# Kernel optimization log

Measured on AMD Instinct MI355X. Metric: run time of the kernel, lower is better.

Reference implementation:

```python
import jax, jax.numpy as jnp
import numpy as np

# dims: O=1 templates/chains, L=384 residues, d_pair=d_bias=128, 4 heads x 32
O, L, DP, DB, H, DH = 1, 384, 128, 128, 4, 32
SCALING = 1.0 / np.sqrt(DH)


def _ln(x, g, b):
    # torch nn.LayerNorm over last dim, eps=1e-5, biased variance
    m = jnp.mean(x, axis=-1, keepdims=True)
    v = jnp.mean((x - m) ** 2, axis=-1, keepdims=True)
    return (x - m) * jax.lax.rsqrt(v + 1e-5) * g + b


def setup_inputs() -> dict:
    key = jax.random.key(0)
    ks = jax.random.split(key, 9)

    def w(k, shape, s=0.02):
        return (jax.random.normal(k, shape) * s).astype(jnp.float32)

    return {
        "pair": jax.random.normal(ks[0], (O, L, L, DP), dtype=jnp.float32),
        "bias": jax.random.normal(ks[1], (O, L, L, DB), dtype=jnp.float32),
        "ln_pair_g": jnp.ones((DP,), jnp.float32),
        "ln_pair_b": jnp.zeros((DP,), jnp.float32),
        "ln_bias_g": jnp.ones((DB,), jnp.float32),
        "ln_bias_b": jnp.zeros((DB,), jnp.float32),
        "Wq": w(ks[2], (H * DH, DP)),  # torch Linear weight layout (out, in)
        "Wk": w(ks[3], (H * DH, DP)),
        "Wv": w(ks[4], (H * DH, DP)),
        "Wb": w(ks[5], (H, DB)),
        "Wg": w(ks[6], (H * DH, DP)),
        "bg": jnp.ones((H * DH,), jnp.float32),
        "Wo": w(ks[7], (DP, H * DH)),
        "bo": w(ks[8], (DP,)),
    }


def reference(pair, bias, ln_pair_g, ln_pair_b, ln_bias_g, ln_bias_b,
              Wq, Wk, Wv, Wb, Wg, bg, Wo, bo):
    # is_row=True: swap the two L axes so attention runs along rows
    p = jnp.transpose(pair, (0, 2, 1, 3))   # [O, L, L, DP]
    bsrc = jnp.transpose(bias, (0, 2, 1, 3))  # [O, L, L, DB]

    p = _ln(p, ln_pair_g, ln_pair_b)
    bsrc = _ln(bsrc, ln_bias_g, ln_bias_b)

    q = (p @ Wq.T).reshape(O, L, L, H, DH) * SCALING
    k = (p @ Wk.T).reshape(O, L, L, H, DH) / L
    v = (p @ Wv.T).reshape(O, L, L, H, DH)
    b = bsrc @ Wb.T                         # [O, L, L, H] pairwise bias
    gate = jax.nn.sigmoid(p @ Wg.T + bg)    # [O, L, L, H*DH]

    # attention scores contracted over the non-attended axial dim n and head dim k
    attn = jnp.einsum('bnihk,bnjhk->bijh', q, k) + b
    attn = jax.nn.softmax(attn, axis=2)     # softmax over j (torch dim=-2)

    out = jnp.einsum('bijh,bnjhd->bnihd', attn, v).reshape(O, L, L, H * DH)
    out = (gate * out) @ Wo.T + bo          # [O, L, L, DP]
    return jnp.transpose(out, (0, 2, 1, 3))  # undo is_row permute
```

## Files before the change

### kernel.cpp

```cpp
#include <hip/hip_runtime.h>
#include <hip/hip_bf16.h>

#define L_DIM 384
#define DPC 128
#define NH 4
#define DHD 32
#define HD 128
#define NROWS (L_DIM*L_DIM)
#define NSPLIT 16

typedef __hip_bfloat16 bf16;
typedef __attribute__((ext_vector_type(8))) short bf8_t;
typedef __attribute__((ext_vector_type(4))) short bf4_t;
typedef __attribute__((ext_vector_type(4))) float f4_t;

__device__ __forceinline__ float bf2f(bf16 x){ return __bfloat162float(x); }
__device__ __forceinline__ bf16 f2bf(float x){ return __float2bfloat16(x); }

union bfu8 { bf8_t v; bf16 h[8]; };

__global__ __launch_bounds__(256) void k_prep(
    const float* __restrict__ Wq, const float* __restrict__ Wk, const float* __restrict__ Wv,
    const float* __restrict__ Wg, const float* __restrict__ Wo,
    bf16* __restrict__ Wqp, bf16* __restrict__ Wkp, bf16* __restrict__ Wvp,
    bf16* __restrict__ Wgp, bf16* __restrict__ Wop)
{
  const int o = blockIdx.x * 256 + threadIdx.x;
  const int j = o & 7, lane = (o >> 3) & 63, ks = (o >> 9) & 3, nt = o >> 11;
  const int src = (nt*16 + (lane & 15))*DPC + ks*32 + (lane >> 4)*8 + j;
  Wqp[o] = f2bf(Wq[src]);
  Wkp[o] = f2bf(Wk[src]);
  Wvp[o] = f2bf(Wv[src]);
  Wgp[o] = f2bf(Wg[src]);
  Wop[o] = f2bf(Wo[src]);
}

__global__ __launch_bounds__(256) void k_bias_proj(
    const float* __restrict__ bias, const float* __restrict__ lng, const float* __restrict__ lnb,
    const float* __restrict__ Wb, float* __restrict__ bscore)
{
  const int tid = threadIdx.x;
  const int wave = tid >> 6, lane = tid & 63;
  const int sub = lane >> 4, l16 = lane & 15, c = l16 * 8;
  const int t = blockIdx.x * 16 + wave * 4 + sub;
  const int j = t / L_DIM, i = t % L_DIM;

  const float4 ga = *(const float4*)&lng[c], gb = *(const float4*)&lng[c+4];
  const float4 ba = *(const float4*)&lnb[c], bb = *(const float4*)&lnb[c+4];
  const float4 xa = *(const float4*)&bias[(size_t)t * DPC + c];
  const float4 xb = *(const float4*)&bias[(size_t)t * DPC + c + 4];

  float s  = xa.x+xa.y+xa.z+xa.w + xb.x+xb.y+xb.z+xb.w;
  float ss = xa.x*xa.x+xa.y*xa.y+xa.z*xa.z+xa.w*xa.w
           + xb.x*xb.x+xb.y*xb.y+xb.z*xb.z+xb.w*xb.w;
  #pragma unroll
  for (int off = 8; off; off >>= 1) { s += __shfl_xor(s, off, 64); ss += __shfl_xor(ss, off, 64); }
  const float mean = s * (1.f/128.f);
  const float var  = ss * (1.f/128.f) - mean*mean;
  const float rstd = rsqrtf(var + 1e-5f);
  float y[8];
  y[0]=(xa.x-mean)*rstd*ga.x+ba.x; y[1]=(xa.y-mean)*rstd*ga.y+ba.y;
  y[2]=(xa.z-mean)*rstd*ga.z+ba.z; y[3]=(xa.w-mean)*rstd*ga.w+ba.w;
  y[4]=(xb.x-mean)*rstd*gb.x+bb.x; y[5]=(xb.y-mean)*rstd*gb.y+bb.y;
  y[6]=(xb.z-mean)*rstd*gb.z+bb.z; y[7]=(xb.w-mean)*rstd*gb.w+bb.w;

  float p[4];
  #pragma unroll
  for (int h = 0; h < 4; ++h) {
    const float4 wa = *(const float4*)&Wb[h*DPC + c];
    const float4 wb4 = *(const float4*)&Wb[h*DPC + c + 4];
    p[h] = y[0]*wa.x + y[1]*wa.y + y[2]*wa.z + y[3]*wa.w
         + y[4]*wb4.x + y[5]*wb4.y + y[6]*wb4.z + y[7]*wb4.w;
    #pragma unroll
    for (int off = 8; off; off >>= 1) p[h] += __shfl_xor(p[h], off, 64);
  }
  if (l16 == 0) {
    #pragma unroll
    for (int h = 0; h < 4; ++h)
      bscore[((size_t)h*L_DIM + i)*L_DIM + j] = p[h];
  }
}

__global__ __launch_bounds__(256) void k_pair_proj(
    const float* __restrict__ pair, const float* __restrict__ lng, const float* __restrict__ lnb,
    const bf16* __restrict__ Wqp, const bf16* __restrict__ Wkp, const bf16* __restrict__ Wvp,
    const bf16* __restrict__ Wgp, const float* __restrict__ bg,
    bf16* __restrict__ qf, bf16* __restrict__ kf, bf16* __restrict__ vf, bf16* __restrict__ gatef)
{
  __shared__ __align__(16) bf16 Sh[5120];
  const int tid = threadIdx.x;
  const int wave = tid >> 6, lane = tid & 63;
  const int n = blockIdx.x / 12, i0 = (blockIdx.x % 12) * 32;
  const int m = lane & 15, q4 = lane >> 4;
  const int rt = wave >> 1, ch = wave & 1;

  {
    const int half = lane >> 5, l32 = lane & 31, c = l32 * 4;
    const float4 g4 = *(const float4*)&lng[c];
    const float4 b4 = *(const float4*)&lnb[c];
    float4 xv[4];
    #pragma unroll
    for (int rr = 0; rr < 4; ++rr) {
      int r = wave*8 + rr*2 + half;
      xv[rr] = *(const float4*)&pair[((size_t)(i0 + r)*L_DIM + n)*DPC + c];
    }
    #pragma unroll
    for (int rr = 0; rr < 4; ++rr) {
      int r = wave*8 + rr*2 + half;
      float s  = xv[rr].x + xv[rr].y + xv[rr].z + xv[rr].w;
      float ss = xv[rr].x*xv[rr].x + xv[rr].y*xv[rr].y + xv[rr].z*xv[rr].z + xv[rr].w*xv[rr].w;
      #pragma unroll
      for (int off = 16; off; off >>= 1) { s += __shfl_xor(s, off, 64); ss += __shfl_xor(ss, off, 64); }
      float mean = s * (1.f/128.f);
      float var  = ss * (1.f/128.f) - mean*mean;
      float rstd = rsqrtf(var + 1e-5f);
      union { bf16 h[4]; bf4_t v; } pk;
      pk.h[0] = f2bf((xv[rr].x-mean)*rstd*g4.x + b4.x);
      pk.h[1] = f2bf((xv[rr].y-mean)*rstd*g4.y + b4.y);
      pk.h[2] = f2bf((xv[rr].z-mean)*rstd*g4.z + b4.z);
      pk.h[3] = f2bf((xv[rr].w-mean)*rstd*g4.w + b4.w);
      *(bf4_t*)&Sh[r*136 + c] = pk.v;
    }
  }
  __syncthreads();

  bf8_t afr[4];
  #pragma unroll
  for (int ks = 0; ks < 4; ++ks)
    afr[ks] = *(const bf8_t*)&Sh[(rt*16 + m)*136 + ks*32 + q4*8];
  __syncthreads();

  const bf16* Ws[4] = {Wqp, Wkp, Wvp, Wgp};
  for (int sel = 0; sel < 4; ++sel) {
    const bf16* Wp = Ws[sel];
    #pragma unroll
    for (int ntl = 0; ntl < 4; ++ntl) {
      const int nt = ch*4 + ntl;
      f4_t acc = {0.f, 0.f, 0.f, 0.f};
      #pragma unroll
      for (int ks = 0; ks < 4; ++ks) {
        bf8_t bfr = *(const bf8_t*)&Wp[(nt*4 + ks)*512 + lane*8];
        acc = __builtin_amdgcn_mfma_f32_16x16x32_bf16(afr[ks], bfr, acc, 0, 0, 0);
      }
      const int col = nt*16 + m;
      if (sel == 2) {
        #pragma unroll
        for (int reg = 0; reg < 4; ++reg)
          Sh[col*40 + rt*16 + q4*4 + reg] = f2bf(acc[reg]);
      } else {
        const float bgv = (sel == 3) ? bg[col] : 0.f;
        #pragma unroll
        for (int reg = 0; reg < 4; ++reg) {
          float v = acc[reg];
          if (sel == 3) v = 1.f / (1.f + __expf(-(v + bgv)));
          Sh[(rt*16 + q4*4 + reg)*136 + col] = f2bf(v);
        }
      }
    }
    __syncthreads();
    if (sel == 2) {
      for (int u = tid; u < 512; u += 256) {
        int ln = u & 63, dt = (u >> 6) & 1, h = u >> 7;
        bf8_t val = *(const bf8_t*)&Sh[(h*32 + dt*16 + (ln&15))*40 + (ln>>4)*8];
        size_t dst = ((((size_t)n*NH + h)*12 + (i0>>5))*2 + dt)*512 + (size_t)ln*8;
        *(bf8_t*)&vf[dst] = val;
      }
    } else {
      for (int u = tid; u < 512; u += 256) {
        int Il = u >> 8, h = (u >> 6) & 3, ln = u & 63;
        bf8_t val = *(const bf8_t*)&Sh[(Il*16 + (ln&15))*136 + h*32 + (ln>>4)*8];
        if (sel == 3) {
          size_t dst = ((((size_t)n*24 + (i0>>4) + Il)*NH + h)*64 + ln)*8;
          *(bf8_t*)&gatef[dst] = val;
        } else {
          bf16* out = (sel == 0) ? qf : kf;
          size_t dst = ((((size_t)n*NH + h)*24 + (i0>>4) + Il)*64 + ln)*8;
          *(bf8_t*)&out[dst] = val;
        }
      }
    }
    __syncthreads();
  }
}

__global__ __launch_bounds__(256) void k_qk(
    const bf16* __restrict__ qf, const bf16* __restrict__ kf, float* __restrict__ Spart)
{
  const int tid = threadIdx.x, wave = tid >> 6, lane = tid & 63;
  const int m = lane & 15, q4 = lane >> 4;
  const int b = blockIdx.x;
  const int ks = b / 36, rem = b % 36;
  const int h = rem / 9, t9 = rem % 9;
  const int i0 = (t9/3)*128, j0 = (t9%3)*128;
  const int wr = (wave >> 1)*64, wc = (wave & 1)*64;

  f4_t acc[4][4];
  #pragma unroll
  for (int a = 0; a < 4; ++a)
    #pragma unroll
    for (int c = 0; c < 4; ++c) acc[a][c] = (f4_t){0.f,0.f,0.f,0.f};

  #pragma unroll 2
  for (int kt = 0; kt < 24; ++kt) {
    const int nIdx = ks*24 + kt;
    const bf16* qb = qf + (((size_t)nIdx*NH + h)*24 + ((i0 + wr) >> 4))*512;
    const bf16* kb = kf + (((size_t)nIdx*NH + h)*24 + ((j0 + wc) >> 4))*512;
    bf8_t af[4], bfr[4];
    #pragma unroll
    for (int x = 0; x < 4; ++x) {
      af[x]  = *(const bf8_t*)&qb[x*512 + lane*8];
      bfr[x] = *(const bf8_t*)&kb[x*512 + lane*8];
    }
    #pragma unroll
    for (int mt = 0; mt < 4; ++mt)
      #pragma unroll
      for (int nt = 0; nt < 4; ++nt)
        acc[mt][nt] = __builtin_amdgcn_mfma_f32_16x16x32_bf16(af[mt], bfr[nt], acc[mt][nt], 0, 0, 0);
  }
  float* Sp = Spart + (size_t)(ks*NH + h)*L_DIM*L_DIM;
  #pragma unroll
  for (int mt = 0; mt < 4; ++mt)
    #pragma unroll
    for (int nt = 0; nt < 4; ++nt)
      #pragma unroll
      for (int reg = 0; reg < 4; ++reg) {
        int i = i0 + wr + mt*16 + q4*4 + reg;
        int j = j0 + wc + nt*16 + m;
        Sp[(size_t)i*L_DIM + j] = acc[mt][nt][reg];
      }
}

__global__ __launch_bounds__(192) void k_softmax(
    const float* __restrict__ Spart, const float* __restrict__ bscore, bf16* __restrict__ attnf)
{
  const int t = threadIdx.x, wave = t >> 6, lane = t & 63;
  const int h = blockIdx.x / L_DIM, i = blockIdx.x % L_DIM;
  const float sc = 0.17677669529663687f / 384.f;
  const size_t off = ((size_t)h*L_DIM + i)*L_DIM + t*2;

  float ax = 0.f, ay = 0.f;
  #pragma unroll
  for (int ksp = 0; ksp < NSPLIT; ++ksp) {
    float2 p = *(const float2*)&Spart[(size_t)ksp*(NH*L_DIM*L_DIM) + off];
    ax += p.x; ay += p.y;
  }
  const float2 bs = *(const float2*)&bscore[off];
  ax = ax*sc + bs.x;
  ay = ay*sc + bs.y;

  __shared__ float redm[3], reds[3];
  float mx = fmaxf(ax, ay);
  #pragma unroll
  for (int o = 32; o; o >>= 1) mx = fmaxf(mx, __shfl_xor(mx, o, 64));
  if (lane == 0) redm[wave] = mx;
  __syncthreads();
  mx = fmaxf(fmaxf(redm[0], redm[1]), redm[2]);
  float ex = __expf(ax - mx), ey = __expf(ay - mx);
  float sm = ex + ey;
  #pragma unroll
  for (int o = 32; o; o >>= 1) sm += __shfl_xor(sm, o, 64);
  if (lane == 0) reds[wave] = sm;
  __syncthreads();
  const float inv = 1.f / (reds[0] + reds[1] + reds[2]);

  const int j = t*2;
  const int I = i >> 4, mm = i & 15, J = j >> 5, q4 = (j >> 3) & 3, jj = j & 7;
  union { bf16 h2[2]; unsigned u; } pk;
  pk.h2[0] = f2bf(ex * inv);
  pk.h2[1] = f2bf(ey * inv);
  size_t a = ((((size_t)h*24 + I)*12 + J)*64 + q4*16 + mm)*8 + jj;
  *(unsigned*)&attnf[a] = pk.u;
}

__global__ __launch_bounds__(256) void k_pv(
    const bf16* __restrict__ attnf, const bf16* __restrict__ vf, const bf16* __restrict__ gatef,
    bf16* __restrict__ goutf)
{
  __shared__ __align__(16) bf16 Cs2[384*40];
  const int tid = threadIdx.x, wave = tid >> 6, lane = tid & 63;
  const int m = lane & 15, q4 = lane >> 4;
  const int n = blockIdx.x >> 2, h = blockIdx.x & 3;

  f4_t acc[6][2];
  #pragma unroll
  for (int a = 0; a < 6; ++a) { acc[a][0] = (f4_t){0,0,0,0}; acc[a][1] = (f4_t){0,0,0,0}; }

  for (int J = 0; J < 12; ++J) {
    const bf16* vb = vf + (((size_t)(n*NH + h)*12 + J)*2)*512;
    bf8_t b0 = *(const bf8_t*)&vb[lane*8];
    bf8_t b1 = *(const bf8_t*)&vb[512 + lane*8];
    #pragma unroll
    for (int mt = 0; mt < 6; ++mt) {
      const int I = wave*6 + mt;
      bf8_t af = *(const bf8_t*)&attnf[(((size_t)h*24 + I)*12 + J)*512 + (size_t)lane*8];
      acc[mt][0] = __builtin_amdgcn_mfma_f32_16x16x32_bf16(af, b0, acc[mt][0], 0, 0, 0);
      acc[mt][1] = __builtin_amdgcn_mfma_f32_16x16x32_bf16(af, b1, acc[mt][1], 0, 0, 0);
    }
  }
  #pragma unroll
  for (int mt = 0; mt < 6; ++mt)
    #pragma unroll
    for (int dt = 0; dt < 2; ++dt)
      #pragma unroll
      for (int reg = 0; reg < 4; ++reg) {
        int i_loc = 16*(wave*6 + mt) + q4*4 + reg;
        Cs2[i_loc*40 + dt*16 + m] = f2bf(acc[mt][dt][reg]);
      }
  __syncthreads();
  #pragma unroll
  for (int it = 0; it < 6; ++it) {
    int u = tid + it*256;
    int I = u >> 6, ln = u & 63;
    bfu8 uc, ug, uo;
    uc.v = *(const bf8_t*)&Cs2[(I*16 + (ln&15))*40 + (ln>>4)*8];
    size_t gidx = ((((size_t)n*24 + I)*NH + h)*64 + ln)*8;
    ug.v = *(const bf8_t*)&gatef[gidx];
    #pragma unroll
    for (int e = 0; e < 8; ++e) uo.h[e] = f2bf(bf2f(uc.h[e]) * bf2f(ug.h[e]));
    *(bf8_t*)&goutf[gidx] = uo.v;
  }
}

__global__ __launch_bounds__(256) void k_out(
    const bf16* __restrict__ goutf, const bf16* __restrict__ Wop, const float* __restrict__ bo,
    float* __restrict__ outp)
{
  __shared__ __align__(16) float Cs[64][132];
  const int tid = threadIdx.x, wave = tid >> 6, lane = tid & 63;
  const int m = lane & 15, q4 = lane >> 4;
  const int n = blockIdx.x / 6, i0 = (blockIdx.x % 6) * 64;

  bf8_t afr[4];
  #pragma unroll
  for (int ks = 0; ks < 4; ++ks)
    afr[ks] = *(const bf8_t*)&goutf[((((size_t)n*24 + (i0>>4) + wave)*NH + ks)*64 + lane)*8];

  #pragma unroll
  for (int nt = 0; nt < 8; ++nt) {
    f4_t acc = {0.f, 0.f, 0.f, 0.f};
    #pragma unroll
    for (int ks = 0; ks < 4; ++ks) {
      bf8_t bfr = *(const bf8_t*)&Wop[(nt*4 + ks)*512 + lane*8];
      acc = __builtin_amdgcn_mfma_f32_16x16x32_bf16(afr[ks], bfr, acc, 0, 0, 0);
    }
    const int col = nt*16 + m;
    const float bov = bo[col];
    #pragma unroll
    for (int reg = 0; reg < 4; ++reg)
      Cs[wave*16 + q4*4 + reg][col] = acc[reg] + bov;
  }
  __syncthreads();
  for (int u = tid; u < 2048; u += 256) {
    int r = u >> 5, c4 = (u & 31) * 4;
    size_t off = ((size_t)(i0 + r)*L_DIM + n)*DPC + c4;
    *(float4*)&outp[off] = *(const float4*)&Cs[r][c4];
  }
}

extern "C" void kernel_launch(void* const* d_in, const int* in_sizes, int n_in,
                              void* d_out, int out_size, void* d_ws, size_t ws_size,
                              hipStream_t stream)
{
  (void)in_sizes; (void)n_in; (void)out_size; (void)ws_size;
  const float* pair = (const float*)d_in[0];
  const float* bias = (const float*)d_in[1];
  const float* lnpg = (const float*)d_in[2];
  const float* lnpb = (const float*)d_in[3];
  const float* lnbg = (const float*)d_in[4];
  const float* lnbb = (const float*)d_in[5];
  const float* Wq   = (const float*)d_in[6];
  const float* Wk   = (const float*)d_in[7];
  const float* Wv   = (const float*)d_in[8];
  const float* Wb   = (const float*)d_in[9];
  const float* Wg   = (const float*)d_in[10];
  const float* bg   = (const float*)d_in[11];
  const float* Wo   = (const float*)d_in[12];
  const float* bo   = (const float*)d_in[13];
  float* outp = (float*)d_out;

  char* ws = (char*)d_ws;
  const size_t SZ = (size_t)NROWS * HD * 2;
  bf16* qfb   = (bf16*)(ws);
  bf16* kfb   = (bf16*)(ws + SZ);
  bf16* vfb   = (bf16*)(ws + 2*SZ);
  bf16* gatef = (bf16*)(ws + 3*SZ);
  float* bscore = (float*)(ws + 4*SZ);
  float* Spart  = (float*)(ws + 4*SZ + (size_t)NH*L_DIM*L_DIM*4);
  bf16*  attnf  = (bf16*)(ws + 4*SZ + (size_t)NH*L_DIM*L_DIM*4 + (size_t)NSPLIT*NH*L_DIM*L_DIM*4);
  char*  wb     = ws + 4*SZ + (size_t)NH*L_DIM*L_DIM*4 + (size_t)NSPLIT*NH*L_DIM*L_DIM*4
                     + (size_t)NH*L_DIM*L_DIM*2;
  bf16* Wqp = (bf16*)(wb);
  bf16* Wkp = (bf16*)(wb + 32768);
  bf16* Wvp = (bf16*)(wb + 65536);
  bf16* Wgp = (bf16*)(wb + 98304);
  bf16* Wop = (bf16*)(wb + 131072);
  bf16* goutf = qfb;

  hipLaunchKernelGGL(k_prep, dim3(64), dim3(256), 0, stream, Wq, Wk, Wv, Wg, Wo,
                     Wqp, Wkp, Wvp, Wgp, Wop);
  hipLaunchKernelGGL(k_bias_proj, dim3(NROWS/16), dim3(256), 0, stream, bias, lnbg, lnbb, Wb, bscore);
  hipLaunchKernelGGL(k_pair_proj, dim3(NROWS/32), dim3(256), 0, stream, pair, lnpg, lnpb,
                     Wqp, Wkp, Wvp, Wgp, bg, qfb, kfb, vfb, gatef);
  hipLaunchKernelGGL(k_qk, dim3(NSPLIT*36), dim3(256), 0, stream, qfb, kfb, Spart);
  hipLaunchKernelGGL(k_softmax, dim3(NH*L_DIM), dim3(192), 0, stream, Spart, bscore, attnf);
  hipLaunchKernelGGL(k_pv, dim3(L_DIM*NH), dim3(256), 0, stream, attnf, vfb, gatef, goutf);
  hipLaunchKernelGGL(k_out, dim3(NROWS/64), dim3(256), 0, stream, goutf, Wop, bo, outp);
}
```

Before: 396.8 us.

## Batch projection stores, prefetch QK fragments, and preload gate in PV kernel

The pair projection kernel now computes Q, K and gate into three separate shared-memory buffers with no barriers between them, then computes V into the reused LN buffer. All global stores are issued in one final pass, which cuts the number of __syncthreads from about eight to three. The QK kernel double-buffers its per-iteration fragment loads so the next tile's global reads overlap the current tile's MFMAs. The PV kernel issues its gate loads before the main loop to hide their latency. In exchange, shared memory per block and register pressure go up, which may lower occupancy.

```diff
diff --git a/kernel.cpp b/kernel.cpp
--- a/kernel.cpp
+++ b/kernel.cpp
@@ -87,7 +87,11 @@
     const bf16* __restrict__ Wgp, const float* __restrict__ bg,
     bf16* __restrict__ qf, bf16* __restrict__ kf, bf16* __restrict__ vf, bf16* __restrict__ gatef)
 {
-  __shared__ __align__(16) bf16 Sh[5120];
+  __shared__ __align__(16) bf16 Sh[5120 + 3*4352];
+  bf16* AsCT = Sh;
+  bf16* Csq  = Sh + 5120;
+  bf16* Csk  = Sh + 5120 + 4352;
+  bf16* Csg  = Sh + 5120 + 2*4352;
   const int tid = threadIdx.x;
   const int wave = tid >> 6, lane = tid & 63;
   const int n = blockIdx.x / 12, i0 = (blockIdx.x % 12) * 32;
@@ -119,7 +123,7 @@
       pk.h[1] = f2bf((xv[rr].y-mean)*rstd*g4.y + b4.y);
       pk.h[2] = f2bf((xv[rr].z-mean)*rstd*g4.z + b4.z);
       pk.h[3] = f2bf((xv[rr].w-mean)*rstd*g4.w + b4.w);
-      *(bf4_t*)&Sh[r*136 + c] = pk.v;
+      *(bf4_t*)&AsCT[r*136 + c] = pk.v;
     }
   }
   __syncthreads();
@@ -127,12 +131,14 @@
   bf8_t afr[4];
   #pragma unroll
   for (int ks = 0; ks < 4; ++ks)
-    afr[ks] = *(const bf8_t*)&Sh[(rt*16 + m)*136 + ks*32 + q4*8];
-  __syncthreads();
-
-  const bf16* Ws[4] = {Wqp, Wkp, Wvp, Wgp};
-  for (int sel = 0; sel < 4; ++sel) {
-    const bf16* Wp = Ws[sel];
+    afr[ks] = *(const bf8_t*)&AsCT[(rt*16 + m)*136 + ks*32 + q4*8];
+
+  const bf16* W3[3] = {Wqp, Wkp, Wgp};
+  bf16* C3[3] = {Csq, Csk, Csg};
+  #pragma unroll
+  for (int s3 = 0; s3 < 3; ++s3) {
+    const bf16* Wp = W3[s3];
+    bf16* Cs = C3[s3];
     #pragma unroll
     for (int ntl = 0; ntl < 4; ++ntl) {
       const int nt = ch*4 + ntl;
@@ -143,43 +149,51 @@
         acc = __builtin_amdgcn_mfma_f32_16x16x32_bf16(afr[ks], bfr, acc, 0, 0, 0);
       }
       const int col = nt*16 + m;
-      if (sel == 2) {
-        #pragma unroll
-        for (int reg = 0; reg < 4; ++reg)
-          Sh[col*40 + rt*16 + q4*4 + reg] = f2bf(acc[reg]);
-      } else {
-        const float bgv = (sel == 3) ? bg[col] : 0.f;
-        #pragma unroll
-        for (int reg = 0; reg < 4; ++reg) {
-          float v = acc[reg];
-          if (sel == 3) v = 1.f / (1.f + __expf(-(v + bgv)));
-          Sh[(rt*16 + q4*4 + reg)*136 + col] = f2bf(v);
-        }
+      const float bgv = (s3 == 2) ? bg[col] : 0.f;
+      #pragma unroll
+      for (int reg = 0; reg < 4; ++reg) {
+        float v = acc[reg];
+        if (s3 == 2) v = 1.f / (1.f + __expf(-(v + bgv)));
+        Cs[(rt*16 + q4*4 + reg)*136 + col] = f2bf(v);
       }
     }
-    __syncthreads();
-    if (sel == 2) {
-      for (int u = tid; u < 512; u += 256) {
-        int ln = u & 63, dt = (u >> 6) & 1, h = u >> 7;
-        bf8_t val = *(const bf8_t*)&Sh[(h*32 + dt*16 + (ln&15))*40 + (ln>>4)*8];
-        size_t dst = ((((size_t)n*NH + h)*12 + (i0>>5))*2 + dt)*512 + (size_t)ln*8;
-        *(bf8_t*)&vf[dst] = val;
-      }
-    } else {
-      for (int u = tid; u < 512; u += 256) {
-        int Il = u >> 8, h = (u >> 6) & 3, ln = u & 63;
-        bf8_t val = *(const bf8_t*)&Sh[(Il*16 + (ln&15))*136 + h*32 + (ln>>4)*8];
-        if (sel == 3) {
-          size_t dst = ((((size_t)n*24 + (i0>>4) + Il)*NH + h)*64 + ln)*8;
-          *(bf8_t*)&gatef[dst] = val;
-        } else {
-          bf16* out = (sel == 0) ? qf : kf;
-          size_t dst = ((((size_t)n*NH + h)*24 + (i0>>4) + Il)*64 + ln)*8;
-          *(bf8_t*)&out[dst] = val;
-        }
-      }
-    }
-    __syncthreads();
+  }
+  __syncthreads();
+
+  #pragma unroll
+  for (int ntl = 0; ntl < 4; ++ntl) {
+    const int nt = ch*4 + ntl;
+    f4_t acc = {0.f, 0.f, 0.f, 0.f};
+    #pragma unroll
+    for (int ks = 0; ks < 4; ++ks) {
+      bf8_t bfr = *(const bf8_t*)&Wvp[(nt*4 + ks)*512 + lane*8];
+      acc = __builtin_amdgcn_mfma_f32_16x16x32_bf16(afr[ks], bfr, acc, 0, 0, 0);
+    }
+    const int col = nt*16 + m;
+    #pragma unroll
+    for (int reg = 0; reg < 4; ++reg)
+      AsCT[col*40 + rt*16 + q4*4 + reg] = f2bf(acc[reg]);
+  }
+  __syncthreads();
+
+  #pragma unroll
+  for (int it = 0; it < 2; ++it) {
+    int u = tid + it*256;
+    {
+      int ln = u & 63, dt = (u >> 6) & 1, h = u >> 7;
+      bf8_t val = *(const bf8_t*)&AsCT[(h*32 + dt*16 + (ln&15))*40 + (ln>>4)*8];
+      size_t dst = ((((size_t)n*NH + h)*12 + (i0>>5))*2 + dt)*512 + (size_t)ln*8;
+      *(bf8_t*)&vf[dst] = val;
+    }
+    {
+      int Il = u >> 8, h = (u >> 6) & 3, ln = u & 63;
+      int lidx = (Il*16 + (ln&15))*136 + h*32 + (ln>>4)*8;
+      size_t dq = ((((size_t)n*NH + h)*24 + (i0>>4) + Il)*64 + ln)*8;
+      *(bf8_t*)&qf[dq] = *(const bf8_t*)&Csq[lidx];
+      *(bf8_t*)&kf[dq] = *(const bf8_t*)&Csk[lidx];
+      size_t dg = ((((size_t)n*24 + (i0>>4) + Il)*NH + h)*64 + ln)*8;
+      *(bf8_t*)&gatef[dg] = *(const bf8_t*)&Csg[lidx];
+    }
   }
 }
 
@@ -200,22 +214,35 @@
     #pragma unroll
     for (int c = 0; c < 4; ++c) acc[a][c] = (f4_t){0.f,0.f,0.f,0.f};
 
+  const bf16* qp = qf + (((size_t)(ks*24)*NH + h)*24 + ((i0 + wr) >> 4))*512 + (size_t)lane*8;
+  const bf16* kp = kf + (((size_t)(ks*24)*NH + h)*24 + ((j0 + wc) >> 4))*512 + (size_t)lane*8;
+  const size_t nstride = (size_t)NH*24*512;
+
+  bf8_t af[4], bfr[4];
+  #pragma unroll
+  for (int x = 0; x < 4; ++x) {
+    af[x]  = *(const bf8_t*)(qp + x*512);
+    bfr[x] = *(const bf8_t*)(kp + x*512);
+  }
   #pragma unroll 2
   for (int kt = 0; kt < 24; ++kt) {
-    const int nIdx = ks*24 + kt;
-    const bf16* qb = qf + (((size_t)nIdx*NH + h)*24 + ((i0 + wr) >> 4))*512;
-    const bf16* kb = kf + (((size_t)nIdx*NH + h)*24 + ((j0 + wc) >> 4))*512;
-    bf8_t af[4], bfr[4];
-    #pragma unroll
-    for (int x = 0; x < 4; ++x) {
-      af[x]  = *(const bf8_t*)&qb[x*512 + lane*8];
-      bfr[x] = *(const bf8_t*)&kb[x*512 + lane*8];
+    bf8_t afn[4], bfn[4];
+    if (kt < 23) {
+      const bf16* qn = qp + (size_t)(kt+1)*nstride;
+      const bf16* kn = kp + (size_t)(kt+1)*nstride;
+      #pragma unroll
+      for (int x = 0; x < 4; ++x) {
+        afn[x] = *(const bf8_t*)(qn + x*512);
+        bfn[x] = *(const bf8_t*)(kn + x*512);
+      }
     }
     #pragma unroll
     for (int mt = 0; mt < 4; ++mt)
       #pragma unroll
       for (int nt = 0; nt < 4; ++nt)
         acc[mt][nt] = __builtin_amdgcn_mfma_f32_16x16x32_bf16(af[mt], bfr[nt], acc[mt][nt], 0, 0, 0);
+    #pragma unroll
+    for (int x = 0; x < 4; ++x) { af[x] = afn[x]; bfr[x] = bfn[x]; }
   }
   float* Sp = Spart + (size_t)(ks*NH + h)*L_DIM*L_DIM;
   #pragma unroll
@@ -281,6 +308,14 @@
   const int m = lane & 15, q4 = lane >> 4;
   const int n = blockIdx.x >> 2, h = blockIdx.x & 3;
 
+  bf8_t ugp[6];
+  #pragma unroll
+  for (int it = 0; it < 6; ++it) {
+    int u = tid + it*256;
+    int I = u >> 6, ln = u & 63;
+    ugp[it] = *(const bf8_t*)&gatef[((((size_t)n*24 + I)*NH + h)*64 + ln)*8];
+  }
+
   f4_t acc[6][2];
   #pragma unroll
   for (int a = 0; a < 6; ++a) { acc[a][0] = (f4_t){0,0,0,0}; acc[a][1] = (f4_t){0,0,0,0}; }
@@ -313,10 +348,10 @@
     int I = u >> 6, ln = u & 63;
     bfu8 uc, ug, uo;
     uc.v = *(const bf8_t*)&Cs2[(I*16 + (ln&15))*40 + (ln>>4)*8];
+    ug.v = ugp[it];
+    #pragma unroll
+    for (int e = 0; e < 8; ++e) uo.h[e] = f2bf(bf2f(uc.h[e]) * bf2f(ug.h[e]));
     size_t gidx = ((((size_t)n*24 + I)*NH + h)*64 + ln)*8;
-    ug.v = *(const bf8_t*)&gatef[gidx];
-    #pragma unroll
-    for (int e = 0; e < 8; ++e) uo.h[e] = f2bf(bf2f(uc.h[e]) * bf2f(ug.h[e]));
     *(bf8_t*)&goutf[gidx] = uo.v;
   }
 }
```

Result: no change. 389.2 us (-1.9%).
